# Kernel tuning notes

Hardware: AMD Instinct MI355X
Metric: run time of the kernel (lower is better)

Reference implementation:

```python
import jax, jax.numpy as jnp
import numpy as np

B, N, DIM, HEADS, RED = 8, 1024, 768, 12, 2
CR = DIM // RED  # 384 reduced channel dim
HD = CR // HEADS  # 32 head dim
EPS = 1e-5


def layer_norm(x, g, b):
    mu = jnp.mean(x, axis=-1, keepdims=True)
    var = jnp.var(x, axis=-1, keepdims=True)
    return (x - mu) * jax.lax.rsqrt(var + EPS) * g + b


def setup_inputs() -> dict:
    key = jax.random.key(0)
    ks = jax.random.split(key, 8)
    s_in = 1.0 / np.sqrt(DIM)
    s_cr = 1.0 / np.sqrt(CR)
    return {
        "x": jax.random.normal(ks[0], (B, N, DIM), dtype=jnp.float32),
        "ln0_g": jnp.ones((DIM,), jnp.float32),
        "ln0_b": jnp.zeros((DIM,), jnp.float32),
        "w_proj": jax.random.normal(ks[1], (CR, DIM), jnp.float32) * s_in,  # conv1x1 -> linear
        "b_proj": jnp.zeros((CR,), jnp.float32),
        "ln1_g": jnp.ones((CR,), jnp.float32),
        "ln1_b": jnp.zeros((CR,), jnp.float32),
        "wq": jax.random.normal(ks[2], (CR, CR), jnp.float32) * s_cr,
        "wk": jax.random.normal(ks[3], (CR, CR), jnp.float32) * s_cr,
        "wv": jax.random.normal(ks[4], (CR, CR), jnp.float32) * s_cr,
    }


def attention(y, wq, wk, wv):
    # y: [B, N, CR]; 1x1 conv == linear on channel dim
    def heads(w):
        return (y @ w.T).reshape(B, N, HEADS, HD).transpose(0, 2, 1, 3)  # [B,H,N,D]
    q, k, v = heads(wq), heads(wk), heads(wv)
    scale = HD ** -0.5
    attn = jax.nn.softmax(jnp.einsum("bhnd,bhmd->bhnm", q, k) * scale, axis=-1)
    out = jnp.einsum("bhnm,bhmd->bhnd", attn, v)  # [B,H,N,D]
    return out.transpose(0, 2, 1, 3).reshape(B, N, CR)


def reference(x, ln0_g, ln0_b, w_proj, b_proj, ln1_g, ln1_b, wq, wk, wv):
    h = layer_norm(x, ln0_g, ln0_b) @ w_proj.T + b_proj  # [B,N,CR]
    y = layer_norm(h, ln1_g, ln1_b)
    return h + attention(y, wq, wk, wv)
```

## Files before the change

kernel.cpp:

```cpp
#include <hip/hip_runtime.h>
#include <math.h>

#define BB 8
#define NN 1024
#define DIM 768
#define HEADS 12
#define CR 384
#define HD 32
#define MROWS (BB*NN)
#define QKVP 1152
#define EPS 1e-5f

typedef __attribute__((ext_vector_type(8))) __bf16 bf16x8;
typedef __attribute__((ext_vector_type(8))) unsigned short u16x8;
typedef __attribute__((ext_vector_type(4))) float f32x4;

__device__ __forceinline__ unsigned short f2bf(float f) {
    unsigned int u = __float_as_uint(f);
    u += 0x7fffu + ((u >> 16) & 1u);
    return (unsigned short)(u >> 16);
}

__device__ __forceinline__ void async_cp16(const unsigned short* g, unsigned short* l) {
    __builtin_amdgcn_global_load_lds(
        (const __attribute__((address_space(1))) unsigned int*)g,
        (__attribute__((address_space(3))) unsigned int*)l, 16, 0, 0);
}

__global__ __launch_bounds__(256) void ln_bf16(
    const float* __restrict__ A, int K,
    const float* __restrict__ g, const float* __restrict__ bt,
    unsigned short* __restrict__ Y)
{
    const int row = blockIdx.x;
    const int t = threadIdx.x;
    const int nv = K >> 2;
    const float* a = A + (size_t)row * K;
    float4 val = make_float4(0.f, 0.f, 0.f, 0.f);
    float s = 0.f, ss = 0.f;
    if (t < nv) {
        val = ((const float4*)a)[t];
        s = val.x + val.y + val.z + val.w;
        ss = val.x * val.x + val.y * val.y + val.z * val.z + val.w * val.w;
    }
    for (int off = 32; off; off >>= 1) {
        s  += __shfl_down(s, off, 64);
        ss += __shfl_down(ss, off, 64);
    }
    __shared__ float rS[4], rSS[4];
    __shared__ float sh_mu, sh_rs;
    int lane = t & 63, w = t >> 6;
    if (lane == 0) { rS[w] = s; rSS[w] = ss; }
    __syncthreads();
    if (t == 0) {
        float S = rS[0] + rS[1] + rS[2] + rS[3];
        float SS = rSS[0] + rSS[1] + rSS[2] + rSS[3];
        float m = S / K;
        sh_mu = m;
        sh_rs = rsqrtf(SS / K - m * m + EPS);
    }
    __syncthreads();
    if (t < nv) {
        float m = sh_mu, r = sh_rs;
        float4 gv = ((const float4*)g)[t];
        float4 bv = ((const float4*)bt)[t];
        ushort4 o = make_ushort4(
            f2bf((val.x - m) * r * gv.x + bv.x),
            f2bf((val.y - m) * r * gv.y + bv.y),
            f2bf((val.z - m) * r * gv.z + bv.z),
            f2bf((val.w - m) * r * gv.w + bv.w));
        ((ushort4*)(Y + (size_t)row * K))[t] = o;
    }
}

__global__ __launch_bounds__(256) void cast_weights(
    const float* __restrict__ wp, const float* __restrict__ wq,
    const float* __restrict__ wk, const float* __restrict__ wv,
    unsigned short* __restrict__ wpo, unsigned short* __restrict__ wqkvo)
{
    int i = blockIdx.x * 256 + threadIdx.x;
    const float* src; unsigned short* dst; int off;
    if (i < 73728) { src = wp; dst = wpo; off = i; }
    else {
        int j = i - 73728;
        int sel = j / 36864; off = j % 36864;
        src = sel == 0 ? wq : (sel == 1 ? wk : wv);
        dst = wqkvo + (size_t)sel * 147456;
    }
    float4 v = ((const float4*)src)[off];
    ushort4 o = make_ushort4(f2bf(v.x), f2bf(v.y), f2bf(v.z), f2bf(v.w));
    ((ushort4*)dst)[off] = o;
}

template<int KD, int BN, bool BF16OUT>
__global__ __launch_bounds__(256) void gemm_mfma(
    const unsigned short* __restrict__ A,
    const unsigned short* __restrict__ W,
    const float* __restrict__ bias,
    void* __restrict__ Cout, int Nn)
{
    constexpr int JT = BN / 32;
    __shared__ unsigned short Asm[128 * 32];
    __shared__ unsigned short Bsm[BN * 32];
    const int t = threadIdx.x;
    const int wave = t >> 6, lane = t & 63;
    const int l15 = lane & 15, quad = lane >> 4;
    const int m0 = blockIdx.y * 128;
    const int n0 = blockIdx.x * BN;
    const int wm = (wave & 1) * 64, wn = (wave >> 1) * (BN / 2);

    const int srow = lane >> 2;
    const int skq  = (lane & 3) * 8;
    const unsigned short* gA0 = A + (size_t)(m0 + wave * 32 + srow) * KD + skq;
    const unsigned short* gB0 = W + (size_t)(n0 + wave * (BN / 4) + srow) * KD + skq;
    unsigned short* lA = Asm + wave * 1024;
    unsigned short* lB = Bsm + wave * (BN * 8);

    f32x4 acc[4][JT];
#pragma unroll
    for (int i = 0; i < 4; i++)
#pragma unroll
        for (int j = 0; j < JT; j++)
            acc[i][j] = (f32x4){0.f, 0.f, 0.f, 0.f};

    for (int k0 = 0; k0 < KD; k0 += 32) {
        __syncthreads();
        async_cp16(gA0 + k0, lA);
        async_cp16(gA0 + (size_t)16 * KD + k0, lA + 512);
        async_cp16(gB0 + k0, lB);
        if (BN == 128) async_cp16(gB0 + (size_t)16 * KD + k0, lB + 512);
        __syncthreads();

        bf16x8 af[4], bf[JT];
#pragma unroll
        for (int i = 0; i < 4; i++)
            af[i] = *(const bf16x8*)(Asm + (wm + i * 16 + l15) * 32 + quad * 8);
#pragma unroll
        for (int j = 0; j < JT; j++)
            bf[j] = *(const bf16x8*)(Bsm + (wn + j * 16 + l15) * 32 + quad * 8);
#pragma unroll
        for (int i = 0; i < 4; i++)
#pragma unroll
            for (int j = 0; j < JT; j++)
                acc[i][j] = __builtin_amdgcn_mfma_f32_16x16x32_bf16(af[i], bf[j], acc[i][j], 0, 0, 0);
    }

    if constexpr (BF16OUT) {
        unsigned short* C = (unsigned short*)Cout;
#pragma unroll
        for (int i = 0; i < 4; i++)
#pragma unroll
            for (int j = 0; j < JT; j++)
#pragma unroll
                for (int reg = 0; reg < 4; reg++) {
                    int row = m0 + wm + i * 16 + quad * 4 + reg;
                    int col = n0 + wn + j * 16 + l15;
                    C[(size_t)row * Nn + col] = f2bf(acc[i][j][reg]);
                }
    } else {
        float* C = (float*)Cout;
        float bv[JT];
#pragma unroll
        for (int j = 0; j < JT; j++) bv[j] = bias[n0 + wn + j * 16 + l15];
#pragma unroll
        for (int i = 0; i < 4; i++)
#pragma unroll
            for (int j = 0; j < JT; j++)
#pragma unroll
                for (int reg = 0; reg < 4; reg++) {
                    int row = m0 + wm + i * 16 + quad * 4 + reg;
                    int col = n0 + wn + j * 16 + l15;
                    C[(size_t)row * Nn + col] = acc[i][j][reg] + bv[j];
                }
    }
}

__global__ __launch_bounds__(256) void attn_mfma(
    const unsigned short* __restrict__ qkv,
    const float* __restrict__ h, float* __restrict__ out)
{
    const int qt = blockIdx.x;
    const int bh = blockIdx.y;
    const int b = bh / HEADS, head = bh % HEADS;
    const int hc = head * HD;
    const int t = threadIdx.x;
    const int wave = t >> 6, lane = t & 63;
    const int l15 = lane & 15, quad = lane >> 4;
    const int q0 = qt * 64;

    __shared__ unsigned short Ks[64 * 40];
    __shared__ unsigned short Vt[32 * 72];
    __shared__ unsigned short Ps[4][16 * 72];

    bf16x8 qa = *(const bf16x8*)(qkv + (size_t)(b * NN + q0 + wave * 16 + l15) * QKVP + hc + quad * 8);

    f32x4 o[2] = {{0.f,0.f,0.f,0.f},{0.f,0.f,0.f,0.f}};
    float lpart[4] = {0.f, 0.f, 0.f, 0.f};
    const float scale = 0.17677669529663687f;

    const int rr = t >> 2, seg = t & 3;
    const unsigned short* gK = qkv + (size_t)(b * NN + rr) * QKVP + CR + hc + seg * 8;
    const unsigned short* gV = qkv + (size_t)(b * NN + lane) * QKVP + 2 * CR + hc + wave * 8;

    for (int kt = 0; kt < 16; kt++) {
        __syncthreads();
        {
            u16x8 kv = *(const u16x8*)(gK + (size_t)kt * 64 * QKVP);
            *(u16x8*)(&Ks[rr * 40 + seg * 8]) = kv;
            u16x8 vv = *(const u16x8*)(gV + (size_t)kt * 64 * QKVP);
#pragma unroll
            for (int j = 0; j < 8; j++)
                Vt[(wave * 8 + j) * 72 + lane] = vv[j];
        }
        __syncthreads();

        f32x4 s[4];
#pragma unroll
        for (int nt = 0; nt < 4; nt++) {
            bf16x8 kb = *(const bf16x8*)(&Ks[(nt * 16 + l15) * 40 + quad * 8]);
            f32x4 z = {0.f, 0.f, 0.f, 0.f};
            s[nt] = __builtin_amdgcn_mfma_f32_16x16x32_bf16(qa, kb, z, 0, 0, 0);
        }

        unsigned short* Pw = Ps[wave];
#pragma unroll
        for (int nt = 0; nt < 4; nt++)
#pragma unroll
            for (int reg = 0; reg < 4; reg++) {
                float e = __expf(s[nt][reg] * scale);
                lpart[reg] += e;
                Pw[(quad * 4 + reg) * 72 + nt * 16 + l15] = f2bf(e);
            }

#pragma unroll
        for (int kk = 0; kk < 2; kk++) {
            bf16x8 pa = *(const bf16x8*)(&Pw[l15 * 72 + kk * 32 + quad * 8]);
#pragma unroll
            for (int nt2 = 0; nt2 < 2; nt2++) {
                bf16x8 vb = *(const bf16x8*)(&Vt[(nt2 * 16 + l15) * 72 + kk * 32 + quad * 8]);
                o[nt2] = __builtin_amdgcn_mfma_f32_16x16x32_bf16(pa, vb, o[nt2], 0, 0, 0);
            }
        }
    }

#pragma unroll
    for (int reg = 0; reg < 4; reg++) {
        float l = lpart[reg];
#pragma unroll
        for (int off = 1; off < 16; off <<= 1) l += __shfl_xor(l, off, 64);
        lpart[reg] = 1.f / l;
    }

#pragma unroll
    for (int nt2 = 0; nt2 < 2; nt2++)
#pragma unroll
        for (int reg = 0; reg < 4; reg++) {
            size_t idx = (size_t)(b * NN + q0 + wave * 16 + quad * 4 + reg) * CR
                       + hc + nt2 * 16 + l15;
            out[idx] = h[idx] + o[nt2][reg] * lpart[reg];
        }
}

extern "C" void kernel_launch(void* const* d_in, const int* in_sizes, int n_in,
                              void* d_out, int out_size, void* d_ws, size_t ws_size,
                              hipStream_t stream) {
    const float* x      = (const float*)d_in[0];
    const float* ln0_g  = (const float*)d_in[1];
    const float* ln0_b  = (const float*)d_in[2];
    const float* w_proj = (const float*)d_in[3];
    const float* b_proj = (const float*)d_in[4];
    const float* ln1_g  = (const float*)d_in[5];
    const float* ln1_b  = (const float*)d_in[6];
    const float* wq     = (const float*)d_in[7];
    const float* wk     = (const float*)d_in[8];
    const float* wv     = (const float*)d_in[9];
    float* out = (float*)d_out;

    char* base = (char*)d_ws;
    unsigned short* qkvb = (unsigned short*)base;
    unsigned short* a0   = (unsigned short*)base;
    float*          hbuf = (float*)(base + 18874368);
    unsigned short* yb   = (unsigned short*)(base + 31457280);
    unsigned short* wp   = (unsigned short*)(base + 37748736);
    unsigned short* wqkv = (unsigned short*)(base + 38338560);

    ln_bf16<<<MROWS, 256, 0, stream>>>(x, DIM, ln0_g, ln0_b, a0);
    cast_weights<<<720, 256, 0, stream>>>(w_proj, wq, wk, wv, wp, wqkv);
    gemm_mfma<DIM, 64, false><<<dim3(CR / 64, MROWS / 128), 256, 0, stream>>>(
        a0, wp, b_proj, hbuf, CR);
    ln_bf16<<<MROWS, 256, 0, stream>>>(hbuf, CR, ln1_g, ln1_b, yb);
    gemm_mfma<CR, 128, true><<<dim3(QKVP / 128, MROWS / 128), 256, 0, stream>>>(
        yb, wqkv, nullptr, qkvb, QKVP);
    attn_mfma<<<dim3(NN / 64, BB * HEADS), 256, 0, stream>>>(qkvb, hbuf, out);
}
```

Measured before the change: 175.8 us.

## Store V transposed and prescale Q in QKV GEMM, drop attention LDS staging

The QKV GEMM epilogue now folds the softmax scale and log2(e) into Q, and writes V in a transposed channel-major buffer. This lets the attention kernel load K and V fragments straight from global memory into registers, with no LDS staging and no per-tile barriers. Attention computes S transposed so each lane holds one query row's scores, uses exp2, and reduces the row sum with two shuffles. Both GEMMs move to 64x64 tiles with a double-buffered async LDS pipeline. The trade-off is more redundant global reads per wave in attention and more, smaller GEMM blocks with less reuse per tile.

```diff
diff --git a/kernel.cpp b/kernel.cpp
--- a/kernel.cpp
+++ b/kernel.cpp
@@ -8,8 +8,8 @@
 #define CR 384
 #define HD 32
 #define MROWS (BB*NN)
-#define QKVP 1152
 #define EPS 1e-5f
+#define SCALE_Q 0.25503486f
 
 typedef __attribute__((ext_vector_type(8))) __bf16 bf16x8;
 typedef __attribute__((ext_vector_type(8))) unsigned short u16x8;
@@ -19,6 +19,10 @@
     unsigned int u = __float_as_uint(f);
     u += 0x7fffu + ((u >> 16) & 1u);
     return (unsigned short)(u >> 16);
+}
+
+__device__ __forceinline__ unsigned int packbf2(float lo, float hi) {
+    return (unsigned int)f2bf(lo) | ((unsigned int)f2bf(hi) << 16);
 }
 
 __device__ __forceinline__ void async_cp16(const unsigned short* g, unsigned short* l) {
@@ -92,91 +96,104 @@
     ((ushort4*)dst)[off] = o;
 }
 
-template<int KD, int BN, bool BF16OUT>
+template<int KD, int MODE>
 __global__ __launch_bounds__(256) void gemm_mfma(
     const unsigned short* __restrict__ A,
     const unsigned short* __restrict__ W,
     const float* __restrict__ bias,
-    void* __restrict__ Cout, int Nn)
+    void* __restrict__ C0, void* __restrict__ C1)
 {
-    constexpr int JT = BN / 32;
-    __shared__ unsigned short Asm[128 * 32];
-    __shared__ unsigned short Bsm[BN * 32];
+    __shared__ unsigned short Asm[2 * 64 * 32];
+    __shared__ unsigned short Bsm[2 * 64 * 32];
     const int t = threadIdx.x;
     const int wave = t >> 6, lane = t & 63;
     const int l15 = lane & 15, quad = lane >> 4;
-    const int m0 = blockIdx.y * 128;
-    const int n0 = blockIdx.x * BN;
-    const int wm = (wave & 1) * 64, wn = (wave >> 1) * (BN / 2);
-
-    const int srow = lane >> 2;
-    const int skq  = (lane & 3) * 8;
-    const unsigned short* gA0 = A + (size_t)(m0 + wave * 32 + srow) * KD + skq;
-    const unsigned short* gB0 = W + (size_t)(n0 + wave * (BN / 4) + srow) * KD + skq;
-    unsigned short* lA = Asm + wave * 1024;
-    unsigned short* lB = Bsm + wave * (BN * 8);
-
-    f32x4 acc[4][JT];
-#pragma unroll
-    for (int i = 0; i < 4; i++)
-#pragma unroll
-        for (int j = 0; j < JT; j++)
-            acc[i][j] = (f32x4){0.f, 0.f, 0.f, 0.f};
-
-    for (int k0 = 0; k0 < KD; k0 += 32) {
+    const int m0 = blockIdx.y * 64;
+    const int n0 = blockIdx.x * 64;
+    const int wm = (wave & 1) * 32, wn = (wave >> 1) * 32;
+
+    const unsigned short* gA = A + (size_t)(m0 + wave * 16 + (lane >> 2)) * KD + (lane & 3) * 8;
+    const unsigned short* gB = W + (size_t)(n0 + wave * 16 + (lane >> 2)) * KD + (lane & 3) * 8;
+    unsigned short* lA = Asm + wave * 512;
+    unsigned short* lB = Bsm + wave * 512;
+
+    constexpr int NIT = KD / 32;
+    async_cp16(gA, lA);
+    async_cp16(gB, lB);
+
+    f32x4 acc[2][2];
+#pragma unroll
+    for (int i = 0; i < 2; i++)
+#pragma unroll
+        for (int j = 0; j < 2; j++) acc[i][j] = (f32x4){0.f, 0.f, 0.f, 0.f};
+
+    for (int it = 0; it < NIT; it++) {
         __syncthreads();
-        async_cp16(gA0 + k0, lA);
-        async_cp16(gA0 + (size_t)16 * KD + k0, lA + 512);
-        async_cp16(gB0 + k0, lB);
-        if (BN == 128) async_cp16(gB0 + (size_t)16 * KD + k0, lB + 512);
-        __syncthreads();
-
-        bf16x8 af[4], bf[JT];
-#pragma unroll
-        for (int i = 0; i < 4; i++)
-            af[i] = *(const bf16x8*)(Asm + (wm + i * 16 + l15) * 32 + quad * 8);
-#pragma unroll
-        for (int j = 0; j < JT; j++)
-            bf[j] = *(const bf16x8*)(Bsm + (wn + j * 16 + l15) * 32 + quad * 8);
-#pragma unroll
-        for (int i = 0; i < 4; i++)
-#pragma unroll
-            for (int j = 0; j < JT; j++)
-                acc[i][j] = __builtin_amdgcn_mfma_f32_16x16x32_bf16(af[i], bf[j], acc[i][j], 0, 0, 0);
-    }
-
-    if constexpr (BF16OUT) {
-        unsigned short* C = (unsigned short*)Cout;
-#pragma unroll
-        for (int i = 0; i < 4; i++)
-#pragma unroll
-            for (int j = 0; j < JT; j++)
+        const int cur = it & 1;
+        if (it + 1 < NIT) {
+            const int nxt = cur ^ 1;
+            async_cp16(gA + (it + 1) * 32, lA + nxt * 2048);
+            async_cp16(gB + (it + 1) * 32, lB + nxt * 2048);
+        }
+        const unsigned short* Ab = Asm + cur * 2048;
+        const unsigned short* Bb = Bsm + cur * 2048;
+        bf16x8 af[2], bfr[2];
+#pragma unroll
+        for (int i = 0; i < 2; i++)
+            af[i] = *(const bf16x8*)(Ab + (wm + i * 16 + l15) * 32 + quad * 8);
+#pragma unroll
+        for (int j = 0; j < 2; j++)
+            bfr[j] = *(const bf16x8*)(Bb + (wn + j * 16 + l15) * 32 + quad * 8);
+#pragma unroll
+        for (int i = 0; i < 2; i++)
+#pragma unroll
+            for (int j = 0; j < 2; j++)
+                acc[i][j] = __builtin_amdgcn_mfma_f32_16x16x32_bf16(af[i], bfr[j], acc[i][j], 0, 0, 0);
+    }
+
+    if constexpr (MODE == 0) {
+        float* C = (float*)C0;
+        float bv[2];
+#pragma unroll
+        for (int j = 0; j < 2; j++) bv[j] = bias[n0 + wn + j * 16 + l15];
+#pragma unroll
+        for (int i = 0; i < 2; i++)
+#pragma unroll
+            for (int j = 0; j < 2; j++)
 #pragma unroll
                 for (int reg = 0; reg < 4; reg++) {
                     int row = m0 + wm + i * 16 + quad * 4 + reg;
                     int col = n0 + wn + j * 16 + l15;
-                    C[(size_t)row * Nn + col] = f2bf(acc[i][j][reg]);
+                    C[(size_t)row * CR + col] = acc[i][j][reg] + bv[j];
                 }
     } else {
-        float* C = (float*)Cout;
-        float bv[JT];
-#pragma unroll
-        for (int j = 0; j < JT; j++) bv[j] = bias[n0 + wn + j * 16 + l15];
-#pragma unroll
-        for (int i = 0; i < 4; i++)
-#pragma unroll
-            for (int j = 0; j < JT; j++)
-#pragma unroll
-                for (int reg = 0; reg < 4; reg++) {
-                    int row = m0 + wm + i * 16 + quad * 4 + reg;
-                    int col = n0 + wn + j * 16 + l15;
-                    C[(size_t)row * Nn + col] = acc[i][j][reg] + bv[j];
+        unsigned short* Cqk = (unsigned short*)C0;
+        unsigned short* Vt  = (unsigned short*)C1;
+#pragma unroll
+        for (int i = 0; i < 2; i++)
+#pragma unroll
+            for (int j = 0; j < 2; j++) {
+                const int colbase = n0 + wn + j * 16;
+                const int token0 = m0 + wm + i * 16 + quad * 4;
+                if (colbase < DIM) {
+                    const float sc = (colbase < CR) ? SCALE_Q : 1.f;
+#pragma unroll
+                    for (int reg = 0; reg < 4; reg++)
+                        Cqk[(size_t)(token0 + reg) * DIM + colbase + l15] = f2bf(acc[i][j][reg] * sc);
+                } else {
+                    const int ch = colbase - DIM + l15;
+                    uint2 pk;
+                    pk.x = packbf2(acc[i][j][0], acc[i][j][1]);
+                    pk.y = packbf2(acc[i][j][2], acc[i][j][3]);
+                    *(uint2*)(Vt + (size_t)ch * MROWS + token0) = pk;
                 }
+            }
     }
 }
 
 __global__ __launch_bounds__(256) void attn_mfma(
-    const unsigned short* __restrict__ qkv,
+    const unsigned short* __restrict__ qk,
+    const unsigned short* __restrict__ vt,
     const float* __restrict__ h, float* __restrict__ out)
 {
     const int qt = blockIdx.x;
@@ -188,77 +205,73 @@
     const int l15 = lane & 15, quad = lane >> 4;
     const int q0 = qt * 64;
 
-    __shared__ unsigned short Ks[64 * 40];
-    __shared__ unsigned short Vt[32 * 72];
     __shared__ unsigned short Ps[4][16 * 72];
-
-    bf16x8 qa = *(const bf16x8*)(qkv + (size_t)(b * NN + q0 + wave * 16 + l15) * QKVP + hc + quad * 8);
+    unsigned short* Pw = Ps[wave];
+
+    bf16x8 qa = *(const bf16x8*)(qk + (size_t)(b * NN + q0 + wave * 16 + l15) * DIM + hc + quad * 8);
+
+    const unsigned short* Kp = qk + (size_t)(b * NN) * DIM + CR + hc + quad * 8;
+    const unsigned short* Vp = vt + (size_t)hc * MROWS + b * NN;
 
     f32x4 o[2] = {{0.f,0.f,0.f,0.f},{0.f,0.f,0.f,0.f}};
-    float lpart[4] = {0.f, 0.f, 0.f, 0.f};
-    const float scale = 0.17677669529663687f;
-
-    const int rr = t >> 2, seg = t & 3;
-    const unsigned short* gK = qkv + (size_t)(b * NN + rr) * QKVP + CR + hc + seg * 8;
-    const unsigned short* gV = qkv + (size_t)(b * NN + lane) * QKVP + 2 * CR + hc + wave * 8;
+    float lpart = 0.f;
 
     for (int kt = 0; kt < 16; kt++) {
-        __syncthreads();
-        {
-            u16x8 kv = *(const u16x8*)(gK + (size_t)kt * 64 * QKVP);
-            *(u16x8*)(&Ks[rr * 40 + seg * 8]) = kv;
-            u16x8 vv = *(const u16x8*)(gV + (size_t)kt * 64 * QKVP);
-#pragma unroll
-            for (int j = 0; j < 8; j++)
-                Vt[(wave * 8 + j) * 72 + lane] = vv[j];
-        }
-        __syncthreads();
+        bf16x8 vb[2][2];
+#pragma unroll
+        for (int kk = 0; kk < 2; kk++)
+#pragma unroll
+            for (int nt2 = 0; nt2 < 2; nt2++)
+                vb[kk][nt2] = *(const bf16x8*)(Vp + (size_t)(nt2 * 16 + l15) * MROWS
+                                               + kt * 64 + kk * 32 + quad * 8);
+        bf16x8 kb[4];
+#pragma unroll
+        for (int nt = 0; nt < 4; nt++)
+            kb[nt] = *(const bf16x8*)(Kp + (size_t)(kt * 64 + nt * 16 + l15) * DIM);
 
         f32x4 s[4];
 #pragma unroll
         for (int nt = 0; nt < 4; nt++) {
-            bf16x8 kb = *(const bf16x8*)(&Ks[(nt * 16 + l15) * 40 + quad * 8]);
             f32x4 z = {0.f, 0.f, 0.f, 0.f};
-            s[nt] = __builtin_amdgcn_mfma_f32_16x16x32_bf16(qa, kb, z, 0, 0, 0);
-        }
-
-        unsigned short* Pw = Ps[wave];
-#pragma unroll
-        for (int nt = 0; nt < 4; nt++)
-#pragma unroll
-            for (int reg = 0; reg < 4; reg++) {
-                float e = __expf(s[nt][reg] * scale);
-                lpart[reg] += e;
-                Pw[(quad * 4 + reg) * 72 + nt * 16 + l15] = f2bf(e);
-            }
+            s[nt] = __builtin_amdgcn_mfma_f32_16x16x32_bf16(kb[nt], qa, z, 0, 0, 0);
+        }
+
+#pragma unroll
+        for (int nt = 0; nt < 4; nt++) {
+            float e0 = __builtin_amdgcn_exp2f(s[nt][0]);
+            float e1 = __builtin_amdgcn_exp2f(s[nt][1]);
+            float e2 = __builtin_amdgcn_exp2f(s[nt][2]);
+            float e3 = __builtin_amdgcn_exp2f(s[nt][3]);
+            lpart += (e0 + e1) + (e2 + e3);
+            uint2 pk;
+            pk.x = packbf2(e0, e1);
+            pk.y = packbf2(e2, e3);
+            *(uint2*)(Pw + l15 * 72 + nt * 16 + quad * 4) = pk;
+        }
 
 #pragma unroll
         for (int kk = 0; kk < 2; kk++) {
-            bf16x8 pa = *(const bf16x8*)(&Pw[l15 * 72 + kk * 32 + quad * 8]);
-#pragma unroll
-            for (int nt2 = 0; nt2 < 2; nt2++) {
-                bf16x8 vb = *(const bf16x8*)(&Vt[(nt2 * 16 + l15) * 72 + kk * 32 + quad * 8]);
-                o[nt2] = __builtin_amdgcn_mfma_f32_16x16x32_bf16(pa, vb, o[nt2], 0, 0, 0);
-            }
-        }
-    }
+            bf16x8 pa = *(const bf16x8*)(Pw + l15 * 72 + kk * 32 + quad * 8);
+#pragma unroll
+            for (int nt2 = 0; nt2 < 2; nt2++)
+                o[nt2] = __builtin_amdgcn_mfma_f32_16x16x32_bf16(pa, vb[kk][nt2], o[nt2], 0, 0, 0);
+        }
+    }
+
+    lpart += __shfl_xor(lpart, 16, 64);
+    lpart += __shfl_xor(lpart, 32, 64);
+    const float linv = 1.f / lpart;
 
 #pragma unroll
     for (int reg = 0; reg < 4; reg++) {
-        float l = lpart[reg];
-#pragma unroll
-        for (int off = 1; off < 16; off <<= 1) l += __shfl_xor(l, off, 64);
-        lpart[reg] = 1.f / l;
-    }
-
-#pragma unroll
-    for (int nt2 = 0; nt2 < 2; nt2++)
-#pragma unroll
-        for (int reg = 0; reg < 4; reg++) {
-            size_t idx = (size_t)(b * NN + q0 + wave * 16 + quad * 4 + reg) * CR
-                       + hc + nt2 * 16 + l15;
-            out[idx] = h[idx] + o[nt2][reg] * lpart[reg];
-        }
+        const float li = __shfl(linv, quad * 4 + reg, 64);
+        const size_t row = (size_t)(b * NN + q0 + wave * 16 + quad * 4 + reg);
+#pragma unroll
+        for (int nt2 = 0; nt2 < 2; nt2++) {
+            size_t idx = row * CR + hc + nt2 * 16 + l15;
+            out[idx] = h[idx] + o[nt2][reg] * li;
+        }
+    }
 }
 
 extern "C" void kernel_launch(void* const* d_in, const int* in_sizes, int n_in,
@@ -277,19 +290,20 @@
     float* out = (float*)d_out;
 
     char* base = (char*)d_ws;
-    unsigned short* qkvb = (unsigned short*)base;
     unsigned short* a0   = (unsigned short*)base;
-    float*          hbuf = (float*)(base + 18874368);
-    unsigned short* yb   = (unsigned short*)(base + 31457280);
+    unsigned short* qkb  = (unsigned short*)base;
+    float*          hbuf = (float*)(base + 12582912);
+    unsigned short* yb   = (unsigned short*)(base + 25165824);
+    unsigned short* vtb  = (unsigned short*)(base + 31457280);
     unsigned short* wp   = (unsigned short*)(base + 37748736);
     unsigned short* wqkv = (unsigned short*)(base + 38338560);
 
     ln_bf16<<<MROWS, 256, 0, stream>>>(x, DIM, ln0_g, ln0_b, a0);
     cast_weights<<<720, 256, 0, stream>>>(w_proj, wq, wk, wv, wp, wqkv);
-    gemm_mfma<DIM, 64, false><<<dim3(CR / 64, MROWS / 128), 256, 0, stream>>>(
-        a0, wp, b_proj, hbuf, CR);
+    gemm_mfma<DIM, 0><<<dim3(CR / 64, MROWS / 64), 256, 0, stream>>>(
+        a0, wp, b_proj, hbuf, nullptr);
     ln_bf16<<<MROWS, 256, 0, stream>>>(hbuf, CR, ln1_g, ln1_b, yb);
-    gemm_mfma<CR, 128, true><<<dim3(QKVP / 128, MROWS / 128), 256, 0, stream>>>(
-        yb, wqkv, nullptr, qkvb, QKVP);
-    attn_mfma<<<dim3(NN / 64, BB * HEADS), 256, 0, stream>>>(qkvb, hbuf, out);
-}
+    gemm_mfma<CR, 1><<<dim3(1152 / 64, MROWS / 64), 256, 0, stream>>>(
+        yb, wqkv, nullptr, qkb, vtb);
+    attn_mfma<<<dim3(NN / 64, BB * HEADS), 256, 0, stream>>>(qkb, vtb, hbuf, out);
+}
```

Result: slower. 270.0 us (+53.6%).
